# Performance work log

Measured on AMD Instinct MI355X. Metric: run time of the kernel, lower is better.

The kernel has to match this reference:

```python
import jax, jax.numpy as jnp
import numpy as np

# Static module config (from Encoder's CropConv layers)
B, CIN, COUT, H, W = 32, 256, 256, 64, 64
K, STRIDE, PAD, DIL = 3, 2, 1, 1
OVERLAP, CENTER = 0, 4


def _build_crop_mask(in_h, out_h, out_w, center_size, overlap):
    """Faithful replica of CropConv's python-loop mask construction,
    including python-slice clamping to L = out_h*out_w."""
    L = out_h * out_w
    crop_start = (in_h - in_h // center_size) // 2 - overlap
    start_idx = in_h * crop_start + crop_start
    crop_size = in_h // center_size + overlap * 2
    not_cropped = crop_start * 2

    def seg_len(a, b):
        # length of python slice [a:b] on an array of length L
        return max(0, min(b, L) - min(a, L))

    segs = []
    for i in range(crop_size):
        if i == 0:
            segs.append(np.ones(seg_len(0, start_idx), bool))
        if i == crop_size - 1:
            segs.append(np.zeros(seg_len(start_idx, start_idx + crop_size), bool))
            segs.append(np.ones(seg_len(start_idx + crop_size, in_h * in_h), bool))
            break
        segs.append(np.zeros(seg_len(start_idx, start_idx + crop_size), bool))
        segs.append(np.ones(seg_len(start_idx + crop_size, start_idx + not_cropped), bool))
        start_idx += in_h
    mask = np.concatenate(segs)
    assert mask.shape[0] == L, (mask.shape[0], L)
    return mask.reshape(out_h, out_w)


def setup_inputs() -> dict:
    key = jax.random.key(0)
    kx, kw = jax.random.split(key)
    x = jax.random.normal(kx, (B, CIN, H, W), dtype=jnp.float32)
    # kaiming_normal(mode='fan_out', nonlinearity='relu'): std = sqrt(2 / (COUT*K*K))
    std = np.sqrt(2.0 / (COUT * K * K)).astype(np.float32)
    weight = jax.random.normal(kw, (COUT, CIN, K, K), dtype=jnp.float32) * std
    return {"x": x, "weight": weight}


def reference(x, weight):
    out_h = (H - K + 2 * PAD) // STRIDE + 1
    out_w = (W - K + 2 * PAD) // STRIDE + 1
    # unfold + matmul == standard convolution; use the efficient fused form
    out = jax.lax.conv_general_dilated(
        x, weight,
        window_strides=(STRIDE, STRIDE),
        padding=[(PAD, PAD), (PAD, PAD)],
        rhs_dilation=(DIL, DIL),
        dimension_numbers=("NCHW", "OIHW", "NCHW"))  # [B, COUT, out_h, out_w]
    mask = jnp.asarray(_build_crop_mask(H, out_h, out_w, CENTER, OVERLAP))
    return jnp.where(mask[None, None, :, :], out, jnp.float32(0.0))
```

## Files before the change

kernel.cpp:

```cpp
#include <hip/hip_runtime.h>


#define B_   32
#define CIN  256
#define COUT 256
#define H_   64
#define W_   64
#define OH   32
#define OW   32

typedef _Float16 f16;
typedef _Float16 half8 __attribute__((ext_vector_type(8)));
typedef float    floatx16 __attribute__((ext_vector_type(16)));

__global__ __launch_bounds__(256) void repack_w_kernel(const float* __restrict__ w,
                                                       f16* __restrict__ rp) {
  int o = blockIdx.x * 256 + threadIdx.x;
  int ci_l = o & 15;
  int tt = o >> 4;
  int co_l = tt & 127; tt >>= 7;
  int khw = tt % 9;    tt /= 9;
  int cc   = tt & 15;  tt >>= 4;
  int co_t = tt;
  int co = co_t * 128 + co_l;
  int ci = cc * 16 + ci_l;
  rp[o] = (f16)w[(co * CIN + ci) * 9 + khw];
}

__global__ __launch_bounds__(256, 2) void conv_mfma_kernel(
    const float* __restrict__ x, const f16* __restrict__ rp,
    float* __restrict__ out) {
  __shared__ f16 ws[9 * 128 * 16];
  __shared__ f16 xs[2 * 9 * 33 * 16];

  const int t    = threadIdx.x;
  const int lane = t & 63;
  const int wave = t >> 6;
  const int wm   = wave >> 1;
  const int wn   = wave & 1;

  const int blk  = blockIdx.x;
  const int b    = blk >> 4;
  const int rem  = blk & 15;
  const int co_t = rem >> 3;
  const int oh0  = (rem & 7) << 2;
  const int ih0  = 2 * oh0 - 1;

  if (t < 144) {
    int r = t >> 4, ci = t & 15;
    xs[((9 + r) * 33 + 0) * 16 + ci] = (f16)0.f;
  }

  floatx16 acc[2][2];
#pragma unroll
  for (int mi = 0; mi < 2; ++mi)
#pragma unroll
    for (int nj = 0; nj < 2; ++nj)
#pragma unroll
      for (int i = 0; i < 16; ++i) acc[mi][nj][i] = 0.f;

  const float* xb  = x + (size_t)b * CIN * H_ * W_;
  const f16*   rpb = rp + (size_t)co_t * (16 * 9 * 128 * 16);

  const int iw = t & 63;
  const int rr = t >> 6;
  const int k0 = (lane >> 5) * 8;
  const int ml = lane & 31;

  for (int cc = 0; cc < 16; ++cc) {
    __syncthreads();
    {
      const half8* src = (const half8*)(rpb + cc * (9 * 128 * 16));
      half8* dst = (half8*)ws;
#pragma unroll
      for (int i = 0; i < 9; ++i) dst[t + i * 256] = src[t + i * 256];
    }
#pragma unroll
    for (int it = 0; it < 3; ++it) {
      int r = rr + it * 4;
      if (r < 9) {
        int ih = ih0 + r;
        const int p   = iw & 1;
        const int idx = (iw + p) >> 1;
#pragma unroll
        for (int g = 0; g < 2; ++g) {
          half8 v;
          if (ih >= 0) {
            const float* xp = xb + ((size_t)(cc * 16 + g * 8) * H_ + ih) * W_ + iw;
#pragma unroll
            for (int c = 0; c < 8; ++c) v[c] = (f16)xp[(size_t)c * H_ * W_];
          } else {
#pragma unroll
            for (int c = 0; c < 8; ++c) v[c] = (f16)0.f;
          }
          *(half8*)&xs[((p * 9 + r) * 33 + idx) * 16 + g * 8] = v;
        }
      }
    }
    __syncthreads();

#pragma unroll
    for (int kh = 0; kh < 3; ++kh) {
#pragma unroll
      for (int kw = 0; kw < 3; ++kw) {
        const int khw = kh * 3 + kw;
        half8 a0 = *(const half8*)&ws[(khw * 128 + wm * 64 + ml) * 16 + k0];
        half8 a1 = *(const half8*)&ws[(khw * 128 + wm * 64 + 32 + ml) * 16 + k0];
        const int p   = (kw & 1) ^ 1;
        const int idx = ml + (kw >> 1);
#pragma unroll
        for (int nj = 0; nj < 2; ++nj) {
          const int r = 2 * (wn * 2 + nj) + kh;
          half8 bf = *(const half8*)&xs[((p * 9 + r) * 33 + idx) * 16 + k0];
          acc[0][nj] = __builtin_amdgcn_mfma_f32_32x32x16_f16(a0, bf, acc[0][nj], 0, 0, 0);
          acc[1][nj] = __builtin_amdgcn_mfma_f32_32x32x16_f16(a1, bf, acc[1][nj], 0, 0, 0);
        }
      }
    }
  }

  const int col = ml;
  const int rowbase = (lane >> 5) * 4;
  float* ob = out + ((size_t)b * COUT + co_t * 128 + wm * 64) * (OH * OW);
#pragma unroll
  for (int mi = 0; mi < 2; ++mi) {
#pragma unroll
    for (int nj = 0; nj < 2; ++nj) {
      const int oh = oh0 + wn * 2 + nj;
#pragma unroll
      for (int r = 0; r < 16; ++r) {
        const int row = mi * 32 + (r & 3) + 8 * (r >> 2) + rowbase;
        ob[(size_t)row * (OH * OW) + oh * OW + col] = acc[mi][nj][r];
      }
    }
  }
}

extern "C" void kernel_launch(void* const* d_in, const int* in_sizes, int n_in,
                              void* d_out, int out_size, void* d_ws, size_t ws_size,
                              hipStream_t stream) {
  const float* x = (const float*)d_in[0];
  const float* w = (const float*)d_in[1];
  float* out = (float*)d_out;
  f16* rp = (f16*)d_ws;

  repack_w_kernel<<<2304, 256, 0, stream>>>(w, rp);
  conv_mfma_kernel<<<512, 256, 0, stream>>>(x, rp, out);
}
```

Before: 241.5 us.

## Double-buffer conv tiles with async weight DMA and larger output tile per block

Restructures the MFMA conv kernel so each block computes 8 output rows instead of 4, doubling per-wave accumulators and halving the grid to 256 blocks. Weights are streamed straight into LDS with global_load_lds into a double buffer, and input channels for the next chunk are prefetched into registers during compute. The LDS layout is split into k-halves to match the new repack order. The aim is to hide global-load latency and to reuse each weight tile across more outputs, at the cost of occupancy (one block per CU, large dynamic LDS, more registers) and only 256 blocks to fill the device.

```diff
diff --git a/kernel.cpp b/kernel.cpp
--- a/kernel.cpp
+++ b/kernel.cpp
@@ -1,136 +1,182 @@
 #include <hip/hip_runtime.h>
 
 
-#define B_   32
 #define CIN  256
-#define COUT 256
 #define H_   64
 #define W_   64
 #define OH   32
 #define OW   32
+#define HW   4096
 
 typedef _Float16 f16;
 typedef _Float16 half8 __attribute__((ext_vector_type(8)));
 typedef float    floatx16 __attribute__((ext_vector_type(16)));
 
+#define WS_CH 18432
+#define XS_CH 17952
+
+typedef const __attribute__((address_space(1))) void g_void;
+typedef __attribute__((address_space(3))) void l_void;
+
 __global__ __launch_bounds__(256) void repack_w_kernel(const float* __restrict__ w,
                                                        f16* __restrict__ rp) {
   int o = blockIdx.x * 256 + threadIdx.x;
-  int ci_l = o & 15;
-  int tt = o >> 4;
-  int co_l = tt & 127; tt >>= 7;
-  int khw = tt % 9;    tt /= 9;
-  int cc   = tt & 15;  tt >>= 4;
-  int co_t = tt;
+  int ci8  = o & 7;
+  int t1   = o >> 3;
+  int co_l = t1 & 127;
+  int t2   = t1 >> 7;
+  int h    = t2 & 1;
+  int t3   = t2 >> 1;
+  int khw  = t3 % 9;
+  int t4   = t3 / 9;
+  int cc   = t4 & 15;
+  int co_t = t4 >> 4;
+  int ci = cc * 16 + h * 8 + ci8;
   int co = co_t * 128 + co_l;
-  int ci = cc * 16 + ci_l;
   rp[o] = (f16)w[(co * CIN + ci) * 9 + khw];
 }
 
-__global__ __launch_bounds__(256, 2) void conv_mfma_kernel(
+__global__ __launch_bounds__(256, 1) void conv_mfma_kernel(
     const float* __restrict__ x, const f16* __restrict__ rp,
     float* __restrict__ out) {
-  __shared__ f16 ws[9 * 128 * 16];
-  __shared__ f16 xs[2 * 9 * 33 * 16];
+  extern __shared__ f16 smem[];
+  f16* wsb = smem;
+  f16* xsb = smem + 2 * WS_CH;
 
   const int t    = threadIdx.x;
   const int lane = t & 63;
   const int wave = t >> 6;
+  const int h    = lane >> 5;
+  const int ml   = lane & 31;
   const int wm   = wave >> 1;
   const int wn   = wave & 1;
 
   const int blk  = blockIdx.x;
-  const int b    = blk >> 4;
-  const int rem  = blk & 15;
-  const int co_t = rem >> 3;
-  const int oh0  = (rem & 7) << 2;
-  const int ih0  = 2 * oh0 - 1;
+  const int co_t = blk >> 7;
+  const int rem  = blk & 127;
+  const int b    = rem >> 2;
+  const int ohg  = rem & 3;
+  const int oh0  = ohg * 8;
+  const int ih0  = oh0 * 2 - 1;
 
-  if (t < 144) {
-    int r = t >> 4, ci = t & 15;
-    xs[((9 + r) * 33 + 0) * 16 + ci] = (f16)0.f;
+  const float* xb  = x  + (size_t)b * CIN * HW;
+  const f16*   rpb = rp + (size_t)co_t * (16 * WS_CH);
+
+  if (t < 68) {
+    int r = t >> 2, hh = t & 1, bufsel = (t >> 1) & 1;
+    half8 z = {};
+    *(half8*)&xsb[bufsel * XS_CH + (((r * 2 + 1) * 2 + hh) * 33 + 0) * 8] = z;
   }
 
-  floatx16 acc[2][2];
+  const int iw  = t & 63;
+  const int p   = iw & 1;
+  const int idx = (iw + p) >> 1;
+
+  floatx16 acc[2][4];
 #pragma unroll
   for (int mi = 0; mi < 2; ++mi)
 #pragma unroll
-    for (int nj = 0; nj < 2; ++nj)
+    for (int nj = 0; nj < 4; ++nj)
 #pragma unroll
       for (int i = 0; i < 16; ++i) acc[mi][nj][i] = 0.f;
 
-  const float* xb  = x + (size_t)b * CIN * H_ * W_;
-  const f16*   rpb = rp + (size_t)co_t * (16 * 9 * 128 * 16);
+  float xr[5][16];
 
-  const int iw = t & 63;
-  const int rr = t >> 6;
-  const int k0 = (lane >> 5) * 8;
-  const int ml = lane & 31;
-
-  for (int cc = 0; cc < 16; ++cc) {
-    __syncthreads();
-    {
-      const half8* src = (const half8*)(rpb + cc * (9 * 128 * 16));
-      half8* dst = (half8*)ws;
+  auto load_x = [&](int c) {
 #pragma unroll
-      for (int i = 0; i < 9; ++i) dst[t + i * 256] = src[t + i * 256];
-    }
+    for (int k = 0; k < 5; ++k) {
+      if (k < 4 || wave == 0) {
+        int r  = wave + 4 * k;
+        int ih = ih0 + r;
+        const float* xp = xb + (size_t)(c * 16) * HW + (size_t)ih * W_ + iw;
+        if (ih >= 0) {
 #pragma unroll
-    for (int it = 0; it < 3; ++it) {
-      int r = rr + it * 4;
-      if (r < 9) {
-        int ih = ih0 + r;
-        const int p   = iw & 1;
-        const int idx = (iw + p) >> 1;
+          for (int j = 0; j < 16; ++j) xr[k][j] = xp[(size_t)j * HW];
+        } else {
 #pragma unroll
-        for (int g = 0; g < 2; ++g) {
-          half8 v;
-          if (ih >= 0) {
-            const float* xp = xb + ((size_t)(cc * 16 + g * 8) * H_ + ih) * W_ + iw;
-#pragma unroll
-            for (int c = 0; c < 8; ++c) v[c] = (f16)xp[(size_t)c * H_ * W_];
-          } else {
-#pragma unroll
-            for (int c = 0; c < 8; ++c) v[c] = (f16)0.f;
-          }
-          *(half8*)&xs[((p * 9 + r) * 33 + idx) * 16 + g * 8] = v;
+          for (int j = 0; j < 16; ++j) xr[k][j] = 0.f;
         }
       }
     }
-    __syncthreads();
+  };
 
+  auto write_x = [&](int buf) {
+    f16* xd = xsb + buf * XS_CH;
+#pragma unroll
+    for (int k = 0; k < 5; ++k) {
+      if (k < 4 || wave == 0) {
+        int r = wave + 4 * k;
+        half8 v0, v1;
+#pragma unroll
+        for (int j = 0; j < 8; ++j) {
+          v0[j] = (f16)xr[k][j];
+          v1[j] = (f16)xr[k][j + 8];
+        }
+        *(half8*)&xd[(((r * 2 + p) * 2 + 0) * 33 + idx) * 8] = v0;
+        *(half8*)&xd[(((r * 2 + p) * 2 + 1) * 33 + idx) * 8] = v1;
+      }
+    }
+  };
+
+  auto dma_w = [&](int c, int buf) {
+    const char* src = (const char*)rpb + (size_t)c * 36864 + wave * 9216 + lane * 16;
+    char* dst = (char*)(wsb + buf * WS_CH) + wave * 9216 + lane * 16;
+#pragma unroll
+    for (int i = 0; i < 9; ++i)
+      __builtin_amdgcn_global_load_lds((g_void*)(src + i * 1024),
+                                       (l_void*)(dst + i * 1024), 16, 0, 0);
+  };
+
+  auto compute = [&](int buf) {
+    const f16* wsc = wsb + buf * WS_CH;
+    const f16* xsc = xsb + buf * XS_CH;
 #pragma unroll
     for (int kh = 0; kh < 3; ++kh) {
 #pragma unroll
       for (int kw = 0; kw < 3; ++kw) {
         const int khw = kh * 3 + kw;
-        half8 a0 = *(const half8*)&ws[(khw * 128 + wm * 64 + ml) * 16 + k0];
-        half8 a1 = *(const half8*)&ws[(khw * 128 + wm * 64 + 32 + ml) * 16 + k0];
-        const int p   = (kw & 1) ^ 1;
-        const int idx = ml + (kw >> 1);
+        half8 a0 = *(const half8*)&wsc[((khw * 2 + h) * 128 + wm * 64 + ml) * 8];
+        half8 a1 = *(const half8*)&wsc[((khw * 2 + h) * 128 + wm * 64 + 32 + ml) * 8];
+        const int pp = (kw & 1) ^ 1;
+        const int ix = ml + (kw >> 1);
 #pragma unroll
-        for (int nj = 0; nj < 2; ++nj) {
-          const int r = 2 * (wn * 2 + nj) + kh;
-          half8 bf = *(const half8*)&xs[((p * 9 + r) * 33 + idx) * 16 + k0];
+        for (int nj = 0; nj < 4; ++nj) {
+          const int r = 2 * (wn * 4 + nj) + kh;
+          half8 bf = *(const half8*)&xsc[(((r * 2 + pp) * 2 + h) * 33 + ix) * 8];
           acc[0][nj] = __builtin_amdgcn_mfma_f32_32x32x16_f16(a0, bf, acc[0][nj], 0, 0, 0);
           acc[1][nj] = __builtin_amdgcn_mfma_f32_32x32x16_f16(a1, bf, acc[1][nj], 0, 0, 0);
         }
       }
     }
+  };
+
+  load_x(0);
+  dma_w(0, 0);
+  write_x(0);
+  __syncthreads();
+
+  for (int cc = 0; cc < 16; ++cc) {
+    const int nb = (cc + 1) & 1;
+    if (cc < 15) {
+      load_x(cc + 1);
+      dma_w(cc + 1, nb);
+    }
+    compute(cc & 1);
+    if (cc < 15) write_x(nb);
+    __syncthreads();
   }
 
-  const int col = ml;
-  const int rowbase = (lane >> 5) * 4;
-  float* ob = out + ((size_t)b * COUT + co_t * 128 + wm * 64) * (OH * OW);
+  float* ob = out + ((size_t)b * 256 + co_t * 128 + wm * 64) * (OH * OW);
+  const int rb4 = h * 4;
 #pragma unroll
   for (int mi = 0; mi < 2; ++mi) {
 #pragma unroll
-    for (int nj = 0; nj < 2; ++nj) {
-      const int oh = oh0 + wn * 2 + nj;
+    for (int nj = 0; nj < 4; ++nj) {
+      const int oh = oh0 + wn * 4 + nj;
 #pragma unroll
       for (int r = 0; r < 16; ++r) {
-        const int row = mi * 32 + (r & 3) + 8 * (r >> 2) + rowbase;
-        ob[(size_t)row * (OH * OW) + oh * OW + col] = acc[mi][nj][r];
+        const int row = mi * 32 + (r & 3) + 8 * (r >> 2) + rb4;
+        ob[(size_t)row * (OH * OW) + oh * OW + ml] = acc[mi][nj][r];
       }
     }
   }
@@ -144,6 +190,10 @@
   float* out = (float*)d_out;
   f16* rp = (f16*)d_ws;
 
+  hipFuncSetAttribute((const void*)conv_mfma_kernel,
+                      hipFuncAttributeMaxDynamicSharedMemorySize,
+                      2 * (WS_CH + XS_CH) * (int)sizeof(f16));
+
   repack_w_kernel<<<2304, 256, 0, stream>>>(w, rp);
-  conv_mfma_kernel<<<512, 256, 0, stream>>>(x, rp, out);
+  conv_mfma_kernel<<<256, 256, 2 * (WS_CH + XS_CH) * sizeof(f16), stream>>>(x, rp, out);
 }
```

Result: no change. 242.8 us (+0.5%).

## Load weights via direct global-to-LDS, vectorize input staging, reorder block mapping

Applied to the files above, without the earlier changes.

Weight tiles are now copied straight from global memory into LDS with global_load_lds, which skips the register round trip. The input staging now reads float4 vectors across 4 channels, replacing scalar strided loads. The LDS layouts for weights and inputs are split by k-half (8 channels) to match both the direct-copy pattern and the MFMA operand fetch. The repack kernel now writes half8 vectors. Block index mapping is changed so the two co tiles sharing the same input are adjacent, which is meant to improve L2 reuse. The risk is LDS bank conflicts from the new half4 scatter stores.

```diff
diff --git a/kernel.cpp b/kernel.cpp
--- a/kernel.cpp
+++ b/kernel.cpp
@@ -1,54 +1,69 @@
 #include <hip/hip_runtime.h>
 
 
-#define B_   32
 #define CIN  256
-#define COUT 256
 #define H_   64
 #define W_   64
 #define OH   32
 #define OW   32
+#define HW   4096
 
 typedef _Float16 f16;
 typedef _Float16 half8 __attribute__((ext_vector_type(8)));
+typedef _Float16 half4 __attribute__((ext_vector_type(4)));
+typedef float    f32x4 __attribute__((ext_vector_type(4)));
 typedef float    floatx16 __attribute__((ext_vector_type(16)));
+
+typedef const __attribute__((address_space(1))) void g_void;
+typedef __attribute__((address_space(3))) void l_void;
 
 __global__ __launch_bounds__(256) void repack_w_kernel(const float* __restrict__ w,
                                                        f16* __restrict__ rp) {
   int o = blockIdx.x * 256 + threadIdx.x;
-  int ci_l = o & 15;
-  int tt = o >> 4;
-  int co_l = tt & 127; tt >>= 7;
-  int khw = tt % 9;    tt /= 9;
-  int cc   = tt & 15;  tt >>= 4;
-  int co_t = tt;
-  int co = co_t * 128 + co_l;
-  int ci = cc * 16 + ci_l;
-  rp[o] = (f16)w[(co * CIN + ci) * 9 + khw];
+  int co_l = o & 127;
+  int t2   = o >> 7;
+  int h    = t2 & 1;
+  int t3   = t2 >> 1;
+  int khw  = t3 % 9;
+  int t4   = t3 / 9;
+  int cc   = t4 & 15;
+  int co_t = t4 >> 4;
+  int co  = co_t * 128 + co_l;
+  int ci0 = cc * 16 + h * 8;
+  half8 v;
+#pragma unroll
+  for (int j = 0; j < 8; ++j) v[j] = (f16)w[(co * CIN + ci0 + j) * 9 + khw];
+  *(half8*)(rp + (size_t)o * 8) = v;
 }
 
 __global__ __launch_bounds__(256, 2) void conv_mfma_kernel(
     const float* __restrict__ x, const f16* __restrict__ rp,
     float* __restrict__ out) {
-  __shared__ f16 ws[9 * 128 * 16];
-  __shared__ f16 xs[2 * 9 * 33 * 16];
+  __shared__ f16 ws[9 * 2 * 128 * 8];
+  __shared__ f16 xs[9 * 2 * 2 * 33 * 8];
 
   const int t    = threadIdx.x;
   const int lane = t & 63;
   const int wave = t >> 6;
+  const int h    = lane >> 5;
+  const int ml   = lane & 31;
   const int wm   = wave >> 1;
   const int wn   = wave & 1;
 
   const int blk  = blockIdx.x;
+  const int co_t = blk & 1;
+  const int ohg  = (blk >> 1) & 7;
   const int b    = blk >> 4;
-  const int rem  = blk & 15;
-  const int co_t = rem >> 3;
-  const int oh0  = (rem & 7) << 2;
+  const int oh0  = ohg * 4;
   const int ih0  = 2 * oh0 - 1;
 
-  if (t < 144) {
-    int r = t >> 4, ci = t & 15;
-    xs[((9 + r) * 33 + 0) * 16 + ci] = (f16)0.f;
+  const float* xb  = x  + (size_t)b * CIN * HW;
+  const f16*   rpb = rp + (size_t)co_t * (16 * 18432);
+
+  if (t < 18) {
+    int r = t >> 1, hh = t & 1;
+    half8 z = {};
+    *(half8*)&xs[(((r * 2 + 1) * 2 + hh) * 33 + 0) * 8] = z;
   }
 
   floatx16 acc[2][2];
@@ -59,41 +74,48 @@
 #pragma unroll
       for (int i = 0; i < 16; ++i) acc[mi][nj][i] = 0.f;
 
-  const float* xb  = x + (size_t)b * CIN * H_ * W_;
-  const f16*   rpb = rp + (size_t)co_t * (16 * 9 * 128 * 16);
-
-  const int iw = t & 63;
-  const int rr = t >> 6;
-  const int k0 = (lane >> 5) * 8;
-  const int ml = lane & 31;
-
   for (int cc = 0; cc < 16; ++cc) {
     __syncthreads();
     {
-      const half8* src = (const half8*)(rpb + cc * (9 * 128 * 16));
-      half8* dst = (half8*)ws;
+      const char* src = (const char*)rpb + (size_t)cc * 36864 + wave * 9216 + lane * 16;
+      char* dst = (char*)ws + wave * 9216 + lane * 16;
 #pragma unroll
-      for (int i = 0; i < 9; ++i) dst[t + i * 256] = src[t + i * 256];
+      for (int i = 0; i < 9; ++i)
+        __builtin_amdgcn_global_load_lds((g_void*)(src + i * 1024),
+                                         (l_void*)(dst + i * 1024), 16, 0, 0);
     }
 #pragma unroll
     for (int it = 0; it < 3; ++it) {
-      int r = rr + it * 4;
-      if (r < 9) {
-        int ih = ih0 + r;
-        const int p   = iw & 1;
-        const int idx = (iw + p) >> 1;
+      int u = t + it * 256;
+      if (u < 576) {
+        int iwq = u & 15;
+        int rg  = u >> 4;
+        int r   = rg % 9;
+        int g   = rg / 9;
+        int ih  = ih0 + r;
+        int ihc = ih < 0 ? 0 : ih;
+        const float* bp = xb + (size_t)(cc * 16 + g * 4) * HW + (size_t)ihc * W_ + iwq * 4;
+        f32x4 v0 = *(const f32x4*)(bp);
+        f32x4 v1 = *(const f32x4*)(bp + HW);
+        f32x4 v2 = *(const f32x4*)(bp + 2 * HW);
+        f32x4 v3 = *(const f32x4*)(bp + 3 * HW);
+        if (ih < 0) {
+          f32x4 z = {0.f, 0.f, 0.f, 0.f};
+          v0 = z; v1 = z; v2 = z; v3 = z;
+        }
+        const int hh  = g >> 1;
+        const int sub = (g & 1) * 4;
 #pragma unroll
-        for (int g = 0; g < 2; ++g) {
-          half8 v;
-          if (ih >= 0) {
-            const float* xp = xb + ((size_t)(cc * 16 + g * 8) * H_ + ih) * W_ + iw;
-#pragma unroll
-            for (int c = 0; c < 8; ++c) v[c] = (f16)xp[(size_t)c * H_ * W_];
-          } else {
-#pragma unroll
-            for (int c = 0; c < 8; ++c) v[c] = (f16)0.f;
-          }
-          *(half8*)&xs[((p * 9 + r) * 33 + idx) * 16 + g * 8] = v;
+        for (int o = 0; o < 4; ++o) {
+          int iw  = iwq * 4 + o;
+          int p   = iw & 1;
+          int idx = (iw + p) >> 1;
+          half4 d;
+          d[0] = (f16)v0[o];
+          d[1] = (f16)v1[o];
+          d[2] = (f16)v2[o];
+          d[3] = (f16)v3[o];
+          *(half4*)&xs[(((r * 2 + p) * 2 + hh) * 33 + idx) * 8 + sub] = d;
         }
       }
     }
@@ -104,14 +126,14 @@
 #pragma unroll
       for (int kw = 0; kw < 3; ++kw) {
         const int khw = kh * 3 + kw;
-        half8 a0 = *(const half8*)&ws[(khw * 128 + wm * 64 + ml) * 16 + k0];
-        half8 a1 = *(const half8*)&ws[(khw * 128 + wm * 64 + 32 + ml) * 16 + k0];
-        const int p   = (kw & 1) ^ 1;
-        const int idx = ml + (kw >> 1);
+        half8 a0 = *(const half8*)&ws[((khw * 2 + h) * 128 + wm * 64 + ml) * 8];
+        half8 a1 = *(const half8*)&ws[((khw * 2 + h) * 128 + wm * 64 + 32 + ml) * 8];
+        const int pp = (kw & 1) ^ 1;
+        const int ix = ml + (kw >> 1);
 #pragma unroll
         for (int nj = 0; nj < 2; ++nj) {
           const int r = 2 * (wn * 2 + nj) + kh;
-          half8 bf = *(const half8*)&xs[((p * 9 + r) * 33 + idx) * 16 + k0];
+          half8 bf = *(const half8*)&xs[(((r * 2 + pp) * 2 + h) * 33 + ix) * 8];
           acc[0][nj] = __builtin_amdgcn_mfma_f32_32x32x16_f16(a0, bf, acc[0][nj], 0, 0, 0);
           acc[1][nj] = __builtin_amdgcn_mfma_f32_32x32x16_f16(a1, bf, acc[1][nj], 0, 0, 0);
         }
@@ -119,9 +141,8 @@
     }
   }
 
-  const int col = ml;
-  const int rowbase = (lane >> 5) * 4;
-  float* ob = out + ((size_t)b * COUT + co_t * 128 + wm * 64) * (OH * OW);
+  float* ob = out + ((size_t)b * 256 + co_t * 128 + wm * 64) * (OH * OW);
+  const int rb4 = h * 4;
 #pragma unroll
   for (int mi = 0; mi < 2; ++mi) {
 #pragma unroll
@@ -129,8 +150,8 @@
       const int oh = oh0 + wn * 2 + nj;
 #pragma unroll
       for (int r = 0; r < 16; ++r) {
-        const int row = mi * 32 + (r & 3) + 8 * (r >> 2) + rowbase;
-        ob[(size_t)row * (OH * OW) + oh * OW + col] = acc[mi][nj][r];
+        const int row = mi * 32 + (r & 3) + 8 * (r >> 2) + rb4;
+        ob[(size_t)row * (OH * OW) + oh * OW + ml] = acc[mi][nj][r];
       }
     }
   }
@@ -144,6 +165,6 @@
   float* out = (float*)d_out;
   f16* rp = (f16*)d_ws;
 
-  repack_w_kernel<<<2304, 256, 0, stream>>>(w, rp);
+  repack_w_kernel<<<288, 256, 0, stream>>>(w, rp);
   conv_mfma_kernel<<<512, 256, 0, stream>>>(x, rp, out);
 }
```

Result: no change. 245.8 us (+1.8%).
